# Kernel tuning notes

Measured on AMD Instinct MI355X. Metric: run time of the kernel, lower is better.

Reference implementation:

```python
import jax, jax.numpy as jnp
import numpy as np

B, T, SD = 16, 512, 64          # batch, action seq len, sample_dim
EMB, HD = 1024, 64              # emb_dim, head_dim
NH = EMB // HD                  # 16 heads
DEPTH, NREG, LAT, FF = 8, 16, 256, 4 * EMB
S = T + NREG                    # total sequence length (actions + registers)


def setup_inputs() -> dict:
    key = jax.random.key(0)
    ks = jax.random.split(key, 16)
    def n(k, shape, scale=0.02):
        return jax.random.normal(k, shape, jnp.float32) * scale
    return {
        "sample": jax.random.normal(ks[0], (B, T, SD), jnp.float32),
        "W_emb": n(ks[1], (SD, EMB)), "b_emb": jnp.zeros((EMB,), jnp.float32),
        "pos": n(ks[2], (T, EMB)),
        "registers": n(ks[3], (NREG, EMB), 1.0),
        "ln1_s": jnp.ones((DEPTH, EMB), jnp.float32), "ln1_b": jnp.zeros((DEPTH, EMB), jnp.float32),
        "W_qkv": n(ks[4], (DEPTH, EMB, 3 * EMB)), "b_qkv": jnp.zeros((DEPTH, 3 * EMB), jnp.float32),
        "W_o": n(ks[5], (DEPTH, EMB, EMB)), "b_o": jnp.zeros((DEPTH, EMB), jnp.float32),
        "ln2_s": jnp.ones((DEPTH, EMB), jnp.float32), "ln2_b": jnp.zeros((DEPTH, EMB), jnp.float32),
        "W_fc1": n(ks[6], (DEPTH, EMB, FF)), "b_fc1": jnp.zeros((DEPTH, FF), jnp.float32),
        "W_fc2": n(ks[7], (DEPTH, FF, EMB)), "b_fc2": jnp.zeros((DEPTH, EMB), jnp.float32),
        "lnf_s": jnp.ones((EMB,), jnp.float32), "lnf_b": jnp.zeros((EMB,), jnp.float32),
        "W_head": n(ks[8], (EMB, LAT)), "b_head": jnp.zeros((LAT,), jnp.float32),
    }


def _ln(x, s, b):
    m = jnp.mean(x, -1, keepdims=True)
    v = jnp.var(x, -1, keepdims=True)
    return (x - m) * jax.lax.rsqrt(v + 1e-5) * s + b


def _causal_last_mask():
    # True = attended to. Actions attend to all actions but NOT registers;
    # registers attend to all actions and causally (incl. self) to registers.
    allowed = jnp.ones((S, S), jnp.bool_)
    allowed = allowed.at[:T, T:].set(False)
    allowed = allowed.at[T:, T:].set(jnp.tril(jnp.ones((NREG, NREG), jnp.bool_)))
    return allowed


def reference(sample, W_emb, b_emb, pos, registers, ln1_s, ln1_b, W_qkv, b_qkv,
              W_o, b_o, ln2_s, ln2_b, W_fc1, b_fc1, W_fc2, b_fc2,
              lnf_s, lnf_b, W_head, b_head):
    # embed + positional add
    x = sample @ W_emb + b_emb + pos[None, :, :]          # [B,T,E]
    # concat registers
    x = jnp.concatenate([x, jnp.broadcast_to(registers, (B, NREG, EMB))], axis=1)  # [B,S,E]
    mask = _causal_last_mask()                             # [S,S]
    scale = 1.0 / jnp.sqrt(jnp.asarray(HD, x.dtype))
    for i in range(DEPTH):
        # pre-LN multi-head attention with structured block mask
        h = _ln(x, ln1_s[i], ln1_b[i])
        qkv = h @ W_qkv[i] + b_qkv[i]
        q, k, v = jnp.split(qkv, 3, axis=-1)
        q = q.reshape(B, S, NH, HD)
        k = k.reshape(B, S, NH, HD)
        v = v.reshape(B, S, NH, HD)
        att = jnp.einsum('bqhd,bkhd->bhqk', q, k) * scale
        att = jnp.where(mask[None, None], att, jnp.finfo(att.dtype).min)
        att = jax.nn.softmax(att, axis=-1)
        o = jnp.einsum('bhqk,bkhd->bqhd', att, v).reshape(B, S, EMB)
        x = x + o @ W_o[i] + b_o[i]
        # pre-LN MLP
        h2 = _ln(x, ln2_s[i], ln2_b[i])
        x = x + jax.nn.gelu(h2 @ W_fc1[i] + b_fc1[i]) @ W_fc2[i] + b_fc2[i]
    x = _ln(x, lnf_s, lnf_b)
    # head applied to register positions only
    return x[:, T:] @ W_head + b_head                      # [B,NREG,LAT]
```

## Files before the change

### kernel.cpp

```cpp
#include <hip/hip_runtime.h>
#include <hip/hip_bf16.h>


typedef unsigned short u16;
typedef __attribute__((ext_vector_type(4))) float f32x4;
typedef __attribute__((ext_vector_type(8))) __bf16 bf16x8;

#define DEV static __device__ __forceinline__

constexpr int Bb = 16, Tt = 512, E = 1024, HD = 64, NHd = 16;
constexpr int DEPTH = 8, NREG = 16, LAT = 256, FF = 4096;
constexpr int S = Tt + NREG;
constexpr int SPAD = 576;
constexpr int MR = Bb * S;
constexpr int ME = Bb * Tt;

DEV u16 f2bf(float f) {
  unsigned u = __builtin_bit_cast(unsigned, f);
  u += 0x7fffu + ((u >> 16) & 1u);
  return (u16)(u >> 16);
}

DEV void gll16(const u16* g, u16* l) {
  __builtin_amdgcn_global_load_lds((const __attribute__((address_space(1))) void*)g,
                                   (__attribute__((address_space(3))) void*)l, 16, 0, 0);
}

enum { M_EMBED, M_QKV, M_OPROJ, M_FC1, M_FC2, M_HEAD };

struct GA {
  const u16* A; const u16* Bt;
  int K, lda, ldb, Nrows, ldc;
  const float* bias; const float* pos;
  float* fout; u16* bout;
  u16 *qp, *kp, *vtp;
};

template<int MODE, int BN>
__global__ __launch_bounds__(256)
void gemm_bt(GA g) {
  constexpr int NI = BN / 32;
  __shared__ __align__(16) u16 As[3][128 * 32];
  __shared__ __align__(16) u16 Bs[3][BN * 32];
  const int tid = threadIdx.x;
  const u16* A  = g.A;
  const u16* Bt = g.Bt;

  int tM, tN;
  {
    const int nwg = gridDim.x * gridDim.y;
    int flat = blockIdx.y * gridDim.x + blockIdx.x;
    const int q = nwg >> 3, r = nwg & 7;
    const int xcd = flat & 7, loc = flat >> 3;
    flat = (xcd < r ? xcd * (q + 1) : r * (q + 1) + (xcd - r) * q) + loc;
    tM = flat / gridDim.x; tN = flat % gridDim.x;
  }

  const int lane = tid & 63, wid = tid >> 6;
  const int wr = wid >> 1, wc = wid & 1;
  const int fr = lane & 15, fg = lane >> 4;

  const int arow = tM * 128 + (tid >> 2);
  int br0 = tN * BN + (tid >> 2);
  if (br0 > g.Nrows - 1) br0 = g.Nrows - 1;
  int br1 = tN * BN + 64 + (tid >> 2);
  if (br1 > g.Nrows - 1) br1 = g.Nrows - 1;
  const int kseg = ((tid & 3) ^ ((tid >> 3) & 3)) * 8;
  const int woff = (tid & 192) * 8;

  const u16* ag0 = A  + (long)arow        * g.lda + kseg;
  const u16* ag1 = A  + (long)(arow + 64) * g.lda + kseg;
  const u16* bg0 = Bt + (long)br0         * g.ldb + kseg;
  const u16* bg1 = Bt + (long)br1         * g.ldb + kseg;

  f32x4 acc[4][NI];
#pragma unroll
  for (int i = 0; i < 4; ++i)
#pragma unroll
    for (int j = 0; j < NI; ++j) acc[i][j] = f32x4{0.f, 0.f, 0.f, 0.f};

#define STAGE(KT, BUF) do {                                   \
    const int _k0 = (KT) << 5;                                \
    gll16(ag0 + _k0, &As[BUF][woff]);                         \
    gll16(ag1 + _k0, &As[BUF][woff + 2048]);                  \
    gll16(bg0 + _k0, &Bs[BUF][woff]);                         \
    if (BN == 128) gll16(bg1 + _k0, &Bs[BUF][woff + 2048]);   \
  } while (0)

  const int nk = g.K >> 5;
  STAGE(0, 0);
  if (nk > 1) STAGE(1, 1);

  const int rsw = (fg ^ ((fr >> 1) & 3)) * 8;

  for (int kt = 0; kt < nk; ++kt) {
    const int cur = kt % 3;
    if (kt < nk - 1) {
      if constexpr (BN == 128) asm volatile("s_waitcnt vmcnt(4)" ::: "memory");
      else                     asm volatile("s_waitcnt vmcnt(3)" ::: "memory");
    } else {
      asm volatile("s_waitcnt vmcnt(0)" ::: "memory");
    }
    __builtin_amdgcn_sched_barrier(0);
    __builtin_amdgcn_s_barrier();
    __builtin_amdgcn_sched_barrier(0);
    if (kt + 2 < nk) STAGE(kt + 2, (kt + 2) % 3);

    bf16x8 af[4], bfr[NI];
#pragma unroll
    for (int mi = 0; mi < 4; ++mi)
      af[mi] = *(const bf16x8*)&As[cur][(wr * 64 + mi * 16 + fr) * 32 + rsw];
#pragma unroll
    for (int ni = 0; ni < NI; ++ni)
      bfr[ni] = *(const bf16x8*)&Bs[cur][(wc * (BN / 2) + ni * 16 + fr) * 32 + rsw];
    __builtin_amdgcn_s_setprio(1);
#pragma unroll
    for (int mi = 0; mi < 4; ++mi)
#pragma unroll
      for (int ni = 0; ni < NI; ++ni)
        acc[mi][ni] = __builtin_amdgcn_mfma_f32_16x16x32_bf16(af[mi], bfr[ni], acc[mi][ni], 0, 0, 0);
    __builtin_amdgcn_s_setprio(0);
  }
#undef STAGE

#pragma unroll
  for (int mi = 0; mi < 4; ++mi)
#pragma unroll
    for (int ni = 0; ni < NI; ++ni)
#pragma unroll
      for (int j = 0; j < 4; ++j) {
        const int row = tM * 128 + wr * 64 + mi * 16 + fg * 4 + j;
        const int col = tN * BN + wc * (BN / 2) + ni * 16 + fr;
        float v = acc[mi][ni][j];
        if (MODE == M_EMBED) {
          const int b = row >> 9, t = row & 511;
          v += g.bias[col] + g.pos[(long)t * E + col];
          g.fout[((long)(b * S + t)) * E + col] = v;
        } else if (MODE == M_QKV) {
          const int b = row / S, s = row - b * S;
          v += g.bias[col];
          const int part = col >> 10, c = col & 1023;
          const int hh = c >> 6, d = c & 63;
          const u16 bf = f2bf(v);
          if (part == 0)      g.qp [((long)((b * NHd + hh) * SPAD + s)) * HD + d] = bf;
          else if (part == 1) g.kp [((long)((b * NHd + hh) * SPAD + s)) * HD + d] = bf;
          else                g.vtp[((long)((b * NHd + hh) * HD   + d)) * SPAD + s] = bf;
        } else if (MODE == M_OPROJ || MODE == M_FC2) {
          const long idx = (long)row * g.ldc + col;
          g.fout[idx] += v + g.bias[col];
        } else if (MODE == M_FC1) {
          v += g.bias[col];
          const float z = 0.7978845608028654f * (v + 0.044715f * v * v * v);
          const float e = __expf(2.f * z);
          const float th = 1.f - 2.f / (e + 1.f);
          g.bout[(long)row * g.ldc + col] = f2bf(0.5f * v * (1.f + th));
        } else if (MODE == M_HEAD) {
          g.fout[(long)row * g.ldc + col] = v + g.bias[col];
        }
      }
}

__global__ __launch_bounds__(256)
void flash_k(const u16* __restrict__ q, const u16* __restrict__ k,
             const u16* __restrict__ vt, u16* __restrict__ o) {
  __shared__ __align__(16) u16 Ks[64 * 64];
  __shared__ __align__(16) u16 Vs[64 * 64];
  __shared__ __align__(16) u16 Ps[4 * 16 * 64];
  const int tid = threadIdx.x;
  const int lane = tid & 63, w = tid >> 6;
  const int fr = lane & 15, fg = lane >> 4;

  int flat = blockIdx.y * 9 + blockIdx.x;
  flat = (flat & 7) * 288 + (flat >> 3);
  const int bh = flat / 9, qt = flat % 9;
  const int q0 = qt * 64;

  const u16* qrow = q + ((long)bh * SPAD + q0 + w * 16 + fr) * HD;
  const bf16x8 qf0 = *(const bf16x8*)(qrow + fg * 8);
  const bf16x8 qf1 = *(const bf16x8*)(qrow + 32 + fg * 8);

  const int srow = lane >> 3, sseg = (lane & 7) * 8;
  const u16* kg = k  + ((long)bh * SPAD + w * 16 + srow) * HD + sseg;
  const u16* vg = vt + ((long)(bh * HD + w * 16 + srow)) * SPAD + sseg;
  u16* lk = Ks + w * 16 * HD;
  u16* lv = Vs + w * 16 * HD;

  float m[4], lsum[4]; f32x4 oa[4];
#pragma unroll
  for (int j = 0; j < 4; ++j) { m[j] = -1e30f; lsum[j] = 0.f; }
#pragma unroll
  for (int n = 0; n < 4; ++n) oa[n] = f32x4{0.f, 0.f, 0.f, 0.f};

  const int nt = (q0 < Tt) ? 8 : 9;
  for (int kt = 0; kt < nt; ++kt) {
    __syncthreads();
    gll16(kg + kt * 64 * HD,          lk);
    gll16(kg + kt * 64 * HD + 8 * HD, lk + 8 * HD);
    gll16(vg + kt * 64,               lv);
    gll16(vg + kt * 64 + 8 * SPAD,    lv + 8 * HD);
    __syncthreads();

    f32x4 sfr[4];
#pragma unroll
    for (int n = 0; n < 4; ++n) {
      const bf16x8 kf0 = *(const bf16x8*)&Ks[(n * 16 + fr) * HD + fg * 8];
      const bf16x8 kf1 = *(const bf16x8*)&Ks[(n * 16 + fr) * HD + 32 + fg * 8];
      sfr[n] = __builtin_amdgcn_mfma_f32_16x16x32_bf16(qf0, kf0, f32x4{0.f,0.f,0.f,0.f}, 0, 0, 0);
      sfr[n] = __builtin_amdgcn_mfma_f32_16x16x32_bf16(qf1, kf1, sfr[n], 0, 0, 0);
    }
    float p[4][4];
#pragma unroll
    for (int j = 0; j < 4; ++j) {
      const int qg = q0 + w * 16 + fg * 4 + j;
      const int vlim = qg < Tt ? Tt : qg + 1;
#pragma unroll
      for (int n = 0; n < 4; ++n) {
        const int col = kt * 64 + n * 16 + fr;
        p[n][j] = (col < vlim) ? sfr[n][j] * 0.125f : -1e30f;
      }
    }
#pragma unroll
    for (int j = 0; j < 4; ++j) {
      float pm = fmaxf(fmaxf(p[0][j], p[1][j]), fmaxf(p[2][j], p[3][j]));
#pragma unroll
      for (int msk = 1; msk <= 8; msk <<= 1) pm = fmaxf(pm, __shfl_xor(pm, msk));
      const float mn = fmaxf(m[j], pm);
      const float corr = __expf(m[j] - mn);
      m[j] = mn;
      float rs = 0.f;
#pragma unroll
      for (int n = 0; n < 4; ++n) { const float e = __expf(p[n][j] - mn); p[n][j] = e; rs += e; }
#pragma unroll
      for (int msk = 1; msk <= 8; msk <<= 1) rs += __shfl_xor(rs, msk);
      lsum[j] = lsum[j] * corr + rs;
#pragma unroll
      for (int n = 0; n < 4; ++n) oa[n][j] *= corr;
    }
#pragma unroll
    for (int j = 0; j < 4; ++j)
#pragma unroll
      for (int n = 0; n < 4; ++n)
        Ps[w * 1024 + (fg * 4 + j) * 64 + n * 16 + fr] = f2bf(p[n][j]);
    __syncthreads();
    const bf16x8 pf0 = *(const bf16x8*)&Ps[w * 1024 + fr * 64 + fg * 8];
    const bf16x8 pf1 = *(const bf16x8*)&Ps[w * 1024 + fr * 64 + 32 + fg * 8];
#pragma unroll
    for (int n = 0; n < 4; ++n) {
      const bf16x8 vf0 = *(const bf16x8*)&Vs[(n * 16 + fr) * HD + fg * 8];
      const bf16x8 vf1 = *(const bf16x8*)&Vs[(n * 16 + fr) * HD + 32 + fg * 8];
      oa[n] = __builtin_amdgcn_mfma_f32_16x16x32_bf16(pf0, vf0, oa[n], 0, 0, 0);
      oa[n] = __builtin_amdgcn_mfma_f32_16x16x32_bf16(pf1, vf1, oa[n], 0, 0, 0);
    }
  }

  const int b = bh >> 4, hh = bh & 15;
#pragma unroll
  for (int j = 0; j < 4; ++j) {
    const int qg = q0 + w * 16 + fg * 4 + j;
    if (qg < S) {
      const float inv = 1.f / lsum[j];
#pragma unroll
      for (int n = 0; n < 4; ++n)
        o[((long)(b * S + qg)) * E + hh * HD + n * 16 + fr] = f2bf(oa[n][j] * inv);
    }
  }
}

__global__ __launch_bounds__(256)
void ln_k(const float* __restrict__ x, const float* __restrict__ sc,
          const float* __restrict__ bi, u16* __restrict__ out, int gather) {
  const int r = blockIdx.x;
  const int srow = gather ? ((r >> 4) * S + Tt + (r & 15)) : r;
  const float4 v = ((const float4*)(x + (long)srow * E))[threadIdx.x];
  float s = v.x + v.y + v.z + v.w;
  float q = v.x * v.x + v.y * v.y + v.z * v.z + v.w * v.w;
#pragma unroll
  for (int o = 32; o; o >>= 1) { s += __shfl_down(s, o); q += __shfl_down(q, o); }
  __shared__ float ps[8];
  if ((threadIdx.x & 63) == 0) { ps[threadIdx.x >> 6] = s; ps[4 + (threadIdx.x >> 6)] = q; }
  __syncthreads();
  s = ps[0] + ps[1] + ps[2] + ps[3];
  q = ps[4] + ps[5] + ps[6] + ps[7];
  const float mean = s * (1.f / E);
  const float rs = rsqrtf(q * (1.f / E) - mean * mean + 1e-5f);
  const int c = threadIdx.x * 4;
  ushort4 o4;
  o4.x = f2bf((v.x - mean) * rs * sc[c + 0] + bi[c + 0]);
  o4.y = f2bf((v.y - mean) * rs * sc[c + 1] + bi[c + 1]);
  o4.z = f2bf((v.z - mean) * rs * sc[c + 2] + bi[c + 2]);
  o4.w = f2bf((v.w - mean) * rs * sc[c + 3] + bi[c + 3]);
  ((ushort4*)(out + (long)r * E))[threadIdx.x] = o4;
}

__global__ __launch_bounds__(256)
void wtrans(const float* __restrict__ src, u16* __restrict__ dst, int R, int C) {
  __shared__ float t[32][33];
  const int c0 = blockIdx.x * 32, r0 = blockIdx.y * 32;
  const int tx = threadIdx.x & 31, ty = threadIdx.x >> 5;
#pragma unroll
  for (int i = 0; i < 32; i += 8) t[ty + i][tx] = src[(long)(r0 + ty + i) * C + c0 + tx];
  __syncthreads();
#pragma unroll
  for (int i = 0; i < 32; i += 8) dst[(long)(c0 + ty + i) * R + r0 + tx] = f2bf(t[tx][ty + i]);
}

__global__ void cvt_bf(const float* __restrict__ in, u16* __restrict__ out, long n) {
  const long i = ((long)blockIdx.x * blockDim.x + threadIdx.x) * 4;
  if (i >= n) return;
  const float4 v = *(const float4*)(in + i);
  ushort4 o; o.x = f2bf(v.x); o.y = f2bf(v.y); o.z = f2bf(v.z); o.w = f2bf(v.w);
  *(ushort4*)(out + i) = o;
}

__global__ void zero_k(float4* p, long n) {
  long i = (long)blockIdx.x * blockDim.x + threadIdx.x;
  const long st = (long)gridDim.x * blockDim.x;
  const float4 z = make_float4(0.f, 0.f, 0.f, 0.f);
  for (; i < n; i += st) p[i] = z;
}

__global__ void reg_copy(const float* __restrict__ regs, float* __restrict__ x) {
  const int b = blockIdx.x >> 4, r = blockIdx.x & 15;
  const float4* sp = (const float4*)(regs + (long)r * E);
  float4* dp = (float4*)(x + ((long)(b * S + Tt + r)) * E);
  dp[threadIdx.x] = sp[threadIdx.x];
}

constexpr long OFF_WQKV = 0L;
constexpr long OFF_WO   = OFF_WQKV + 3072L * 1024 * 2;
constexpr long OFF_WFC1 = OFF_WO   + 1024L * 1024 * 2;
constexpr long OFF_WFC2 = OFF_WFC1 + 4096L * 1024 * 2;
constexpr long OFF_WEMB = OFF_WFC2 + 1024L * 4096 * 2;
constexpr long OFF_WHEAD= OFF_WEMB + 1024L * 64 * 2;
constexpr long OFF_SMP  = OFF_WHEAD+ 256L * 1024 * 2;
constexpr long OFF_X    = OFF_SMP  + (long)ME * 64 * 2;
constexpr long OFF_H    = OFF_X    + (long)MR * E * 4;
constexpr long OFF_Q    = OFF_H    + (long)MR * E * 2;
constexpr long OFF_K    = OFF_Q    + 256L * SPAD * HD * 2;
constexpr long OFF_VT   = OFF_K    + 256L * SPAD * HD * 2;
constexpr long OFF_O    = OFF_VT   + 256L * SPAD * HD * 2;
constexpr long OFF_HF   = OFF_O    + (long)MR * FF * 2;
constexpr long WS_NEED  = OFF_HF   + 256L * 1024 * 2;

extern "C" void kernel_launch(void* const* d_in, const int* in_sizes, int n_in,
                              void* d_out, int out_size, void* d_ws, size_t ws_size,
                              hipStream_t stream) {
  if (ws_size < (size_t)WS_NEED) return;

  const float* sample = (const float*)d_in[0];
  const float* W_emb  = (const float*)d_in[1];
  const float* b_emb  = (const float*)d_in[2];
  const float* pos    = (const float*)d_in[3];
  const float* regs   = (const float*)d_in[4];
  const float* ln1_s  = (const float*)d_in[5];
  const float* ln1_b  = (const float*)d_in[6];
  const float* W_qkv  = (const float*)d_in[7];
  const float* b_qkv  = (const float*)d_in[8];
  const float* W_o    = (const float*)d_in[9];
  const float* b_o    = (const float*)d_in[10];
  const float* ln2_s  = (const float*)d_in[11];
  const float* ln2_b  = (const float*)d_in[12];
  const float* W_fc1  = (const float*)d_in[13];
  const float* b_fc1  = (const float*)d_in[14];
  const float* W_fc2  = (const float*)d_in[15];
  const float* b_fc2  = (const float*)d_in[16];
  const float* lnf_s  = (const float*)d_in[17];
  const float* lnf_b  = (const float*)d_in[18];
  const float* W_head = (const float*)d_in[19];
  const float* b_head = (const float*)d_in[20];

  char* w = (char*)d_ws;
  u16* wqkvT = (u16*)(w + OFF_WQKV);
  u16* woT   = (u16*)(w + OFF_WO);
  u16* wfc1T = (u16*)(w + OFF_WFC1);
  u16* wfc2T = (u16*)(w + OFF_WFC2);
  u16* wembT = (u16*)(w + OFF_WEMB);
  u16* wheadT= (u16*)(w + OFF_WHEAD);
  u16* smp   = (u16*)(w + OFF_SMP);
  float* x   = (float*)(w + OFF_X);
  u16* h     = (u16*)(w + OFF_H);
  u16* qp    = (u16*)(w + OFF_Q);
  u16* kp    = (u16*)(w + OFF_K);
  u16* vtp   = (u16*)(w + OFF_VT);
  u16* o     = (u16*)(w + OFF_O);
  u16* a1    = (u16*)(w + OFF_O);
  u16* hf    = (u16*)(w + OFF_HF);

  wtrans<<<dim3(32, 2, 1), 256, 0, stream>>>(W_emb,  wembT, 64, 1024);
  wtrans<<<dim3(8, 32, 1), 256, 0, stream>>>(W_head, wheadT, 1024, 256);
  cvt_bf<<<dim3(512), 256, 0, stream>>>(sample, smp, (long)ME * 64);
  zero_k<<<dim3(2048), 256, 0, stream>>>((float4*)qp, (3L * 256 * SPAD * HD * 2) / 16);

  {
    GA g{}; g.A = smp; g.Bt = wembT; g.K = 64; g.lda = 64; g.ldb = 64;
    g.Nrows = E; g.bias = b_emb; g.pos = pos; g.fout = x;
    gemm_bt<M_EMBED, 64><<<dim3(16, 64, 1), 256, 0, stream>>>(g);
  }
  reg_copy<<<dim3(256), 256, 0, stream>>>(regs, x);

  for (int L = 0; L < DEPTH; ++L) {
    wtrans<<<dim3(96, 32, 1),  256, 0, stream>>>(W_qkv + (long)L * 1024 * 3072, wqkvT, 1024, 3072);
    wtrans<<<dim3(32, 32, 1),  256, 0, stream>>>(W_o   + (long)L * 1024 * 1024, woT,   1024, 1024);
    wtrans<<<dim3(128, 32, 1), 256, 0, stream>>>(W_fc1 + (long)L * 1024 * 4096, wfc1T, 1024, 4096);
    wtrans<<<dim3(32, 128, 1), 256, 0, stream>>>(W_fc2 + (long)L * 4096 * 1024, wfc2T, 4096, 1024);

    ln_k<<<dim3(MR), 256, 0, stream>>>(x, ln1_s + L * E, ln1_b + L * E, h, 0);
    {
      GA g{}; g.A = h; g.Bt = wqkvT;
      g.K = 1024; g.lda = 1024; g.ldb = 1024; g.Nrows = 3072;
      g.bias = b_qkv + L * 3072; g.qp = qp; g.kp = kp; g.vtp = vtp;
      gemm_bt<M_QKV, 128><<<dim3(24, 66, 1), 256, 0, stream>>>(g);
    }
    flash_k<<<dim3(9, 256, 1), 256, 0, stream>>>(qp, kp, vtp, o);
    {
      GA g{}; g.A = o; g.Bt = woT;
      g.K = 1024; g.lda = 1024; g.ldb = 1024; g.Nrows = 1024; g.ldc = 1024;
      g.bias = b_o + L * E; g.fout = x;
      gemm_bt<M_OPROJ, 128><<<dim3(8, 66, 1), 256, 0, stream>>>(g);
    }
    ln_k<<<dim3(MR), 256, 0, stream>>>(x, ln2_s + L * E, ln2_b + L * E, h, 0);
    {
      GA g{}; g.A = h; g.Bt = wfc1T;
      g.K = 1024; g.lda = 1024; g.ldb = 1024; g.Nrows = 4096; g.ldc = 4096;
      g.bias = b_fc1 + L * FF; g.bout = a1;
      gemm_bt<M_FC1, 128><<<dim3(32, 66, 1), 256, 0, stream>>>(g);
    }
    {
      GA g{}; g.A = a1; g.Bt = wfc2T;
      g.K = 4096; g.lda = 4096; g.ldb = 4096; g.Nrows = 1024; g.ldc = 1024;
      g.bias = b_fc2 + L * E; g.fout = x;
      gemm_bt<M_FC2, 128><<<dim3(8, 66, 1), 256, 0, stream>>>(g);
    }
  }

  ln_k<<<dim3(256), 256, 0, stream>>>(x, lnf_s, lnf_b, hf, 1);
  {
    GA g{}; g.A = hf; g.Bt = wheadT; g.K = 1024; g.lda = 1024; g.ldb = 1024;
    g.Nrows = LAT; g.ldc = LAT; g.bias = b_head; g.fout = (float*)d_out;
    gemm_bt<M_HEAD, 128><<<dim3(2, 2, 1), 256, 0, stream>>>(g);
  }
}
```

Measured before the change: 3.895 ms.

## Deepen GEMM LDS pipeline to four stages and swizzle flash-attention LDS tiles

The GEMM moves from three to four LDS buffers, prefetching three k-tiles ahead with adjusted vmcnt waits so global load latency is hidden more fully. The flash-attention kernel XOR-swizzles the K, V and P tiles in LDS to reduce bank conflicts on the 16-byte fragment reads. It also replaces the block-wide barrier after the per-wave P write with a local lgkmcnt wait, since each wave only reads its own P tile. The extra GEMM buffer raises LDS use per block, which may lower occupancy.

```diff
diff --git a/kernel.cpp b/kernel.cpp
--- a/kernel.cpp
+++ b/kernel.cpp
@@ -40,8 +40,8 @@
 __global__ __launch_bounds__(256)
 void gemm_bt(GA g) {
   constexpr int NI = BN / 32;
-  __shared__ __align__(16) u16 As[3][128 * 32];
-  __shared__ __align__(16) u16 Bs[3][BN * 32];
+  __shared__ __align__(16) u16 As[4][128 * 32];
+  __shared__ __align__(16) u16 Bs[4][BN * 32];
   const int tid = threadIdx.x;
   const u16* A  = g.A;
   const u16* Bt = g.Bt;
@@ -90,21 +90,24 @@
   const int nk = g.K >> 5;
   STAGE(0, 0);
   if (nk > 1) STAGE(1, 1);
+  if (nk > 2) STAGE(2, 2);
 
   const int rsw = (fg ^ ((fr >> 1) & 3)) * 8;
+  constexpr int LPS = (BN == 128) ? 4 : 3;
 
   for (int kt = 0; kt < nk; ++kt) {
-    const int cur = kt % 3;
-    if (kt < nk - 1) {
-      if constexpr (BN == 128) asm volatile("s_waitcnt vmcnt(4)" ::: "memory");
-      else                     asm volatile("s_waitcnt vmcnt(3)" ::: "memory");
+    const int cur = kt & 3;
+    if (kt < nk - 2) {
+      asm volatile("s_waitcnt vmcnt(%0)" :: "i"(2 * LPS) : "memory");
+    } else if (kt == nk - 2) {
+      asm volatile("s_waitcnt vmcnt(%0)" :: "i"(LPS) : "memory");
     } else {
       asm volatile("s_waitcnt vmcnt(0)" ::: "memory");
     }
     __builtin_amdgcn_sched_barrier(0);
     __builtin_amdgcn_s_barrier();
     __builtin_amdgcn_sched_barrier(0);
-    if (kt + 2 < nk) STAGE(kt + 2, (kt + 2) % 3);
+    if (kt + 3 < nk) STAGE(kt + 3, (kt + 3) & 3);
 
     bf16x8 af[4], bfr[NI];
 #pragma unroll
@@ -179,11 +182,14 @@
   const bf16x8 qf0 = *(const bf16x8*)(qrow + fg * 8);
   const bf16x8 qf1 = *(const bf16x8*)(qrow + 32 + fg * 8);
 
-  const int srow = lane >> 3, sseg = (lane & 7) * 8;
+  const int srow = lane >> 3;
+  const int sseg = (((lane & 7) ^ (srow & 7)) * 8);
   const u16* kg = k  + ((long)bh * SPAD + w * 16 + srow) * HD + sseg;
   const u16* vg = vt + ((long)(bh * HD + w * 16 + srow)) * SPAD + sseg;
   u16* lk = Ks + w * 16 * HD;
   u16* lv = Vs + w * 16 * HD;
+
+  const int frm = fr & 7;
 
   float m[4], lsum[4]; f32x4 oa[4];
 #pragma unroll
@@ -203,8 +209,8 @@
     f32x4 sfr[4];
 #pragma unroll
     for (int n = 0; n < 4; ++n) {
-      const bf16x8 kf0 = *(const bf16x8*)&Ks[(n * 16 + fr) * HD + fg * 8];
-      const bf16x8 kf1 = *(const bf16x8*)&Ks[(n * 16 + fr) * HD + 32 + fg * 8];
+      const bf16x8 kf0 = *(const bf16x8*)&Ks[(n * 16 + fr) * HD + ((fg ^ frm) * 8)];
+      const bf16x8 kf1 = *(const bf16x8*)&Ks[(n * 16 + fr) * HD + (((fg + 4) ^ frm) * 8)];
       sfr[n] = __builtin_amdgcn_mfma_f32_16x16x32_bf16(qf0, kf0, f32x4{0.f,0.f,0.f,0.f}, 0, 0, 0);
       sfr[n] = __builtin_amdgcn_mfma_f32_16x16x32_bf16(qf1, kf1, sfr[n], 0, 0, 0);
     }
@@ -237,17 +243,22 @@
       for (int n = 0; n < 4; ++n) oa[n][j] *= corr;
     }
 #pragma unroll
-    for (int j = 0; j < 4; ++j)
-#pragma unroll
-      for (int n = 0; n < 4; ++n)
-        Ps[w * 1024 + (fg * 4 + j) * 64 + n * 16 + fr] = f2bf(p[n][j]);
-    __syncthreads();
-    const bf16x8 pf0 = *(const bf16x8*)&Ps[w * 1024 + fr * 64 + fg * 8];
-    const bf16x8 pf1 = *(const bf16x8*)&Ps[w * 1024 + fr * 64 + 32 + fg * 8];
+    for (int j = 0; j < 4; ++j) {
+      const int r = fg * 4 + j;
+#pragma unroll
+      for (int n = 0; n < 4; ++n) {
+        const int gr = 2 * n + (fr >> 3);
+        Ps[w * 1024 + r * 64 + ((gr ^ (r & 7)) * 8) + frm] = f2bf(p[n][j]);
+      }
+    }
+    asm volatile("s_waitcnt lgkmcnt(0)" ::: "memory");
+    __builtin_amdgcn_sched_barrier(0);
+    const bf16x8 pf0 = *(const bf16x8*)&Ps[w * 1024 + fr * 64 + ((fg ^ frm) * 8)];
+    const bf16x8 pf1 = *(const bf16x8*)&Ps[w * 1024 + fr * 64 + (((fg + 4) ^ frm) * 8)];
 #pragma unroll
     for (int n = 0; n < 4; ++n) {
-      const bf16x8 vf0 = *(const bf16x8*)&Vs[(n * 16 + fr) * HD + fg * 8];
-      const bf16x8 vf1 = *(const bf16x8*)&Vs[(n * 16 + fr) * HD + 32 + fg * 8];
+      const bf16x8 vf0 = *(const bf16x8*)&Vs[(n * 16 + fr) * HD + ((fg ^ frm) * 8)];
+      const bf16x8 vf1 = *(const bf16x8*)&Vs[(n * 16 + fr) * HD + (((fg + 4) ^ frm) * 8)];
       oa[n] = __builtin_amdgcn_mfma_f32_16x16x32_bf16(pf0, vf0, oa[n], 0, 0, 0);
       oa[n] = __builtin_amdgcn_mfma_f32_16x16x32_bf16(pf1, vf1, oa[n], 0, 0, 0);
     }
```

Result: slower. 4.807 ms (+23.4%).
